# Kernel tuning notes

Hardware: AMD Instinct MI355X
Metric: run time of the kernel (lower is better)

The kernel has to match this reference:

```python
import jax, jax.numpy as jnp
import numpy as np

B, S, H, NH, HD = 2, 2048, 1024, 16, 64
THETA = 10000.0


def setup_inputs() -> dict:
    key = jax.random.key(0)
    k1, k2, k3, k4, k5 = jax.random.split(key, 5)
    hidden_states = jax.random.normal(k1, (B, S, H), dtype=jnp.float32)
    # RoPE tables, interleaved-pair layout: [c0,c0,c1,c1,...] along head_dim
    inv_freq = 1.0 / (THETA ** (jnp.arange(0, HD, 2, dtype=jnp.float32) / HD))
    t = jnp.arange(S, dtype=jnp.float32)
    freqs = jnp.outer(t, inv_freq)                      # [S, HD//2]
    freqs_cos = jnp.repeat(jnp.cos(freqs), 2, axis=-1)  # [S, HD]
    freqs_sin = jnp.repeat(jnp.sin(freqs), 2, axis=-1)  # [S, HD]
    position_ids = jnp.arange(S, dtype=jnp.int32)
    w = 0.02
    Wq = jax.random.normal(k2, (H, H), dtype=jnp.float32) * w
    Wk = jax.random.normal(k3, (H, H), dtype=jnp.float32) * w
    Wv = jax.random.normal(k4, (H, H), dtype=jnp.float32) * w
    Wo = jax.random.normal(k5, (H, H), dtype=jnp.float32) * w
    return {"hidden_states": hidden_states, "freqs_cos": freqs_cos,
            "freqs_sin": freqs_sin, "position_ids": position_ids,
            "Wq": Wq, "Wk": Wk, "Wv": Wv, "Wo": Wo}


def _rotate_half_interleaved(x):
    # stack([-x[..., 1::2], x[..., ::2]], -1).reshape_as(x)
    xe = x.reshape(x.shape[:-1] + (HD // 2, 2))
    return jnp.stack([-xe[..., 1], xe[..., 0]], axis=-1).reshape(x.shape)


def reference(hidden_states, freqs_cos, freqs_sin, position_ids, Wq, Wk, Wv, Wo):
    b, s, _ = hidden_states.shape
    # QKV projections (torch Linear: y = x @ W.T), split into heads [b, nh, s, hd]
    q = jnp.einsum('bsh,oh->bso', hidden_states, Wq).reshape(b, s, NH, HD).transpose(0, 2, 1, 3)
    k = jnp.einsum('bsh,oh->bso', hidden_states, Wk).reshape(b, s, NH, HD).transpose(0, 2, 1, 3)
    v = jnp.einsum('bsh,oh->bso', hidden_states, Wv).reshape(b, s, NH, HD).transpose(0, 2, 1, 3)
    cos = freqs_cos[position_ids][None, None]  # [1, 1, s, hd]
    sin = freqs_sin[position_ids][None, None]
    rq = _rotate_half_interleaved(q)
    # NOTE: faithful to source bug — rotate_half_k is built from q, not k
    q = q * cos + rq * sin
    k = k * cos + rq * sin
    # causal SDPA, scale = 1/sqrt(head_dim)
    scores = jnp.einsum('bhqd,bhkd->bhqk', q, k) / jnp.sqrt(jnp.float32(HD))
    causal = jnp.tril(jnp.ones((s, s), dtype=bool))
    scores = jnp.where(causal, scores, jnp.float32(-1e30))
    attn = jax.nn.softmax(scores, axis=-1)
    out = jnp.einsum('bhqk,bhkd->bhqd', attn, v)
    out = out.transpose(0, 2, 1, 3).reshape(b, s, H)
    return jnp.einsum('bsh,oh->bso', out, Wo)
```

## Files before the change

kernel.cpp:

```cpp
#include <hip/hip_runtime.h>
#include <stdint.h>

#define BB 2
#define SS 2048
#define HH 1024
#define NHH 16
#define HDD 64

typedef short bf16s;
typedef __attribute__((ext_vector_type(8))) short short8;
typedef __attribute__((ext_vector_type(4))) short short4v;
typedef __attribute__((ext_vector_type(2))) short short2v;
typedef __attribute__((ext_vector_type(4))) float f32x4;
typedef _Float16 half4v __attribute__((ext_vector_type(4)));
typedef _Float16 half8v __attribute__((ext_vector_type(8)));
typedef __fp16 fp16x2 __attribute__((ext_vector_type(2)));

__device__ inline short f2bf(float f) {
  union { float f; uint32_t u; } v; v.f = f;
  uint32_t r = (v.u + 0x7fffu + ((v.u >> 16) & 1u)) >> 16;
  return (short)r;
}
__device__ inline float bf2f(short h) {
  union { uint32_t u; float f; } v; v.u = ((uint32_t)(uint16_t)h) << 16;
  return v.f;
}

__device__ __forceinline__ float exp2_raw(float x) {
  float r;
  asm("v_exp_f32 %0, %1\n\ts_nop 0" : "=v"(r) : "v"(x));
  return r;
}

__device__ inline void gld_lds16(const void* g, void* l) {
  __builtin_amdgcn_global_load_lds((const __attribute__((address_space(1))) void*)g,
                                   (__attribute__((address_space(3))) void*)l, 16, 0, 0);
}

__device__ inline void stv(short* C, size_t i, float v) { C[i] = f2bf(v); }
__device__ inline void stv(float* C, size_t i, float v) { C[i] = v; }

__device__ inline f32x4 mfma_k32(short8 a, short8 b, f32x4 c) {
  return __builtin_amdgcn_mfma_f32_16x16x32_bf16(a, b, c, 0, 0, 0);
}
__device__ inline f32x4 mfma_k32(half8v a, half8v b, f32x4 c) {
  return __builtin_amdgcn_mfma_f32_16x16x32_f16(a, b, c, 0, 0, 0);
}
template <typename ET> struct ftr;
template <> struct ftr<short>     { using v8 = short8; };
template <> struct ftr<_Float16>  { using v8 = half8v; };

__global__ __launch_bounds__(256) void convert_all(
    const float* __restrict__ x, const float* __restrict__ Wq,
    const float* __restrict__ Wk, const float* __restrict__ Wv,
    const float* __restrict__ Wo, bf16s* __restrict__ xb,
    bf16s* __restrict__ wqkv, _Float16* __restrict__ wof) {
  const long M1 = 1024L * 1024L;
  long e = (long)(blockIdx.x * blockDim.x + threadIdx.x) * 4;
  if (e < 7 * M1) {
    const float* src; bf16s* dst;
    if (e < 4 * M1)      { src = x  + e;            dst = xb   + e; }
    else if (e < 5 * M1) { src = Wq + (e - 4 * M1); dst = wqkv + (e - 4 * M1); }
    else if (e < 6 * M1) { src = Wk + (e - 5 * M1); dst = wqkv + (e - 4 * M1); }
    else                 { src = Wv + (e - 6 * M1); dst = wqkv + (e - 4 * M1); }
    float4 v = *(const float4*)src;
    short4v o;
    o.x = f2bf(v.x); o.y = f2bf(v.y); o.z = f2bf(v.z); o.w = f2bf(v.w);
    *(short4v*)dst = o;
  } else {
    float4 v = *(const float4*)(Wo + (e - 7 * M1));
    half4v o;
    o.x = (_Float16)v.x; o.y = (_Float16)v.y;
    o.z = (_Float16)v.z; o.w = (_Float16)v.w;
    *(half4v*)(wof + (e - 7 * M1)) = o;
  }
}

template <typename ET, typename OT, int MT>
__global__ __launch_bounds__(256) void gemm_bt(
    const ET* __restrict__ A, const ET* __restrict__ Bm,
    OT* __restrict__ C, int K, int ldc) {
  using V8 = typename ftr<ET>::v8;
  __shared__ __align__(16) ET As[MT * 32 * 64];
  __shared__ __align__(16) ET Bs[128 * 64];
  const int tid = threadIdx.x;
  const int lane = tid & 63, w = tid >> 6;
  const int quad = lane >> 4, mcol = lane & 15;
  const int bm = blockIdx.y * (MT * 32), bn = blockIdx.x * 128;
  const int wm = (w >> 1) * (MT * 16), wn = (w & 1) * 64;
  f32x4 acc[MT][4] = {};
  const int nkt = K >> 6;
  for (int kt = 0; kt < nkt; ++kt) {
    __syncthreads();
#pragma unroll
    for (int i = 0; i < MT; ++i) {
      int seg = (i * 4 + w) * 512;
      int flat = seg + lane * 8;
      int row = flat >> 6;
      int cpos = (flat >> 3) & 7;
      int cs = cpos ^ (row & 7);
      gld_lds16(A + (size_t)(bm + row) * K + kt * 64 + cs * 8, &As[seg]);
    }
#pragma unroll
    for (int i = 0; i < 4; ++i) {
      int seg = (i * 4 + w) * 512;
      int flat = seg + lane * 8;
      int row = flat >> 6;
      int cpos = (flat >> 3) & 7;
      int cs = cpos ^ (row & 7);
      gld_lds16(Bm + (size_t)(bn + row) * K + kt * 64 + cs * 8, &Bs[seg]);
    }
    __syncthreads();
#pragma unroll
    for (int ks = 0; ks < 2; ++ks) {
      V8 af[MT], bf[4];
#pragma unroll
      for (int mt = 0; mt < MT; ++mt) {
        int row = wm + mt * 16 + mcol;
        int cs = (ks * 4 + quad) ^ (row & 7);
        af[mt] = *(const V8*)&As[row * 64 + cs * 8];
      }
#pragma unroll
      for (int nt = 0; nt < 4; ++nt) {
        int row = wn + nt * 16 + mcol;
        int cs = (ks * 4 + quad) ^ (row & 7);
        bf[nt] = *(const V8*)&Bs[row * 64 + cs * 8];
      }
#pragma unroll
      for (int mt = 0; mt < MT; ++mt)
#pragma unroll
        for (int nt = 0; nt < 4; ++nt)
          acc[mt][nt] = mfma_k32(af[mt], bf[nt], acc[mt][nt]);
    }
  }
#pragma unroll
  for (int mt = 0; mt < MT; ++mt)
#pragma unroll
    for (int nt = 0; nt < 4; ++nt) {
      int r0 = bm + wm + mt * 16 + quad * 4;
      int c = bn + wn + nt * 16 + mcol;
#pragma unroll
      for (int r = 0; r < 4; ++r)
        stv(C, (size_t)(r0 + r) * ldc + c, acc[mt][nt][r]);
    }
}

__global__ __launch_bounds__(256) void postproc(
    const bf16s* __restrict__ qkv, const float* __restrict__ fcos,
    const float* __restrict__ fsin, const int* __restrict__ pos,
    bf16s* __restrict__ Q, bf16s* __restrict__ Kc, _Float16* __restrict__ Vt) {
  const float LOG2E = 1.4426950408889634f;
  const int st = blockIdx.x, bh = blockIdx.y;
  const int b = bh >> 4, h = bh & 15;
  const int tid = threadIdx.x;
  const int m0 = b * 2048 + st * 64;
  {
    const int row = tid >> 2, pc = tid & 3;
    const int s = st * 64 + row;
    const int p = pos[s];
    const bf16s* qp = qkv + (size_t)(m0 + row) * 3072 + h * 64 + pc * 16;
    short8 qv[2] = { *(const short8*)qp, *(const short8*)(qp + 8) };
    short8 kv[2] = { *(const short8*)(qp + 1024), *(const short8*)(qp + 1032) };
    const float* cp = fcos + (size_t)p * 64 + pc * 16;
    const float* sp = fsin + (size_t)p * 64 + pc * 16;
    short8 qo[2], ko[2];
#pragma unroll
    for (int hf = 0; hf < 2; ++hf)
#pragma unroll
      for (int j = 0; j < 4; ++j) {
        float c = cp[hf * 8 + 2 * j], sn = sp[hf * 8 + 2 * j];
        float q0 = bf2f(qv[hf][2 * j]), q1 = bf2f(qv[hf][2 * j + 1]);
        float k0 = bf2f(kv[hf][2 * j]), k1 = bf2f(kv[hf][2 * j + 1]);
        qo[hf][2 * j]     = f2bf((q0 * c - q1 * sn) * 0.125f);
        qo[hf][2 * j + 1] = f2bf((q1 * c + q0 * sn) * 0.125f);
        ko[hf][2 * j]     = f2bf((k0 * c - q1 * sn) * LOG2E);
        ko[hf][2 * j + 1] = f2bf((k1 * c + q0 * sn) * LOG2E);
      }
    size_t o = ((size_t)bh * 2048 + s) * 64 + pc * 16;
    *(short8*)&Q[o] = qo[0];  *(short8*)&Q[o + 8] = qo[1];
    *(short8*)&Kc[o] = ko[0]; *(short8*)&Kc[o + 8] = ko[1];
  }
  __shared__ __align__(16) _Float16 T[64 * 72];
#pragma unroll
  for (int p2 = 0; p2 < 2; ++p2) {
    int sl = p2 * 32 + (tid >> 3);
    int ch = tid & 7;
    short8 v = *(const short8*)&qkv[(size_t)(m0 + sl) * 3072 + 2048 + h * 64 + ch * 8];
#pragma unroll
    for (int j = 0; j < 8; ++j) T[(ch * 8 + j) * 72 + sl] = (_Float16)bf2f(v[j]);
  }
  __syncthreads();
#pragma unroll
  for (int p2 = 0; p2 < 2; ++p2) {
    int dl = p2 * 32 + (tid >> 3);
    int ch = tid & 7;
    half8v v = *(const half8v*)&T[dl * 72 + ch * 8];
    *(half8v*)&Vt[((size_t)bh * 64 + dl) * 2048 + st * 64 + ch * 8] = v;
  }
}

template <bool DOB>
__device__ __forceinline__ void step2(
    const bf16s* __restrict__ Ks, const _Float16* __restrict__ Vp,
    const short8* bqA, const short8* bqB,
    f32x4* OA, f32x4* OB, float& lA, float& lB,
    bool diagA, bool diagB, int w, int quad, int col) {
  f32x4 sA[4], sB[4];
#pragma unroll
  for (int t = 0; t < 4; ++t) {
    f32x4 a = {}, bb = {};
#pragma unroll
    for (int ks = 0; ks < 2; ++ks) {
      int krow = t * 16 + col;
      int cs = (ks * 4 + quad) ^ (krow & 7);
      short8 af = *(const short8*)&Ks[krow * 64 + cs * 8];
      a = __builtin_amdgcn_mfma_f32_16x16x32_bf16(af, bqA[ks], a, 0, 0, 0);
      if (DOB) bb = __builtin_amdgcn_mfma_f32_16x16x32_bf16(af, bqB[ks], bb, 0, 0, 0);
    }
    sA[t] = a;
    if (DOB) sB[t] = bb;
  }
  if (diagA) {
#pragma unroll
    for (int t = 0; t < 4; ++t)
#pragma unroll
      for (int r = 0; r < 4; ++r)
        if (t * 16 + quad * 4 + r > w * 16 + col) sA[t][r] = -1e30f;
  }
  if (DOB && diagB) {
#pragma unroll
    for (int t = 0; t < 4; ++t)
#pragma unroll
      for (int r = 0; r < 4; ++r)
        if (t * 16 + quad * 4 + r > w * 16 + col) sB[t][r] = -1e30f;
  }
  half4v paA[4], paB[4];
#pragma unroll
  for (int t = 0; t < 4; ++t) {
    {
      float p0 = exp2_raw(sA[t][0]), p1 = exp2_raw(sA[t][1]);
      float p2 = exp2_raw(sA[t][2]), p3 = exp2_raw(sA[t][3]);
      lA += (p0 + p1) + (p2 + p3);
      union { fp16x2 h2[2]; half4v h4; } u;
      u.h2[0] = __builtin_amdgcn_cvt_pkrtz(p0, p1);
      u.h2[1] = __builtin_amdgcn_cvt_pkrtz(p2, p3);
      paA[t] = u.h4;
    }
    if (DOB) {
      float p0 = exp2_raw(sB[t][0]), p1 = exp2_raw(sB[t][1]);
      float p2 = exp2_raw(sB[t][2]), p3 = exp2_raw(sB[t][3]);
      lB += (p0 + p1) + (p2 + p3);
      union { fp16x2 h2[2]; half4v h4; } u;
      u.h2[0] = __builtin_amdgcn_cvt_pkrtz(p0, p1);
      u.h2[1] = __builtin_amdgcn_cvt_pkrtz(p2, p3);
      paB[t] = u.h4;
    }
  }
#pragma unroll
  for (int dt = 0; dt < 4; ++dt) {
    int vrow = dt * 16 + col;
    const _Float16* vp = &Vp[vrow * 72 + (quad ^ (vrow & 3)) * 16];
    union { half8v v8; half4v v4[2]; } a01, a23;
    a01.v8 = *(const half8v*)vp;
    a23.v8 = *(const half8v*)(vp + 8);
    half4v bv[4] = { a01.v4[0], a01.v4[1], a23.v4[0], a23.v4[1] };
#pragma unroll
    for (int t = 0; t < 4; ++t) {
      OA[dt] = __builtin_amdgcn_mfma_f32_16x16x16f16(paA[t], bv[t], OA[dt], 0, 0, 0);
      if (DOB) OB[dt] = __builtin_amdgcn_mfma_f32_16x16x16f16(paB[t], bv[t], OB[dt], 0, 0, 0);
    }
  }
}

__global__ __launch_bounds__(256) void attn(
    const bf16s* __restrict__ Q, const bf16s* __restrict__ Kb,
    const _Float16* __restrict__ Vt, _Float16* __restrict__ O) {
  __shared__ __align__(16) bf16s Ks[2][64 * 64];
  __shared__ __align__(16) _Float16 Vp[2][64 * 72];
  const int bh = blockIdx.y;
  const int tid = threadIdx.x, lane = tid & 63, w = tid >> 6;
  const int quad = lane >> 4, col = lane & 15;
  const size_t base = (size_t)bh * 2048 * 64;
  const _Float16* vbase = Vt + (size_t)bh * 64 * 2048;
  const int b = bh >> 4, h = bh & 15;
  const int x = blockIdx.x;
  const int qbA = 31 - x, qbB = x;

  short8 bqA[2], bqB[2];
  {
    const int qrA = qbA * 64 + w * 16 + col;
    const int qrB = qbB * 64 + w * 16 + col;
#pragma unroll
    for (int ks = 0; ks < 2; ++ks) {
      bqA[ks] = *(const short8*)&Q[base + (size_t)qrA * 64 + ks * 32 + quad * 8];
      bqB[ks] = *(const short8*)&Q[base + (size_t)qrB * 64 + ks * 32 + quad * 8];
    }
  }
  f32x4 OA[4] = {}, OB[4] = {};
  float lA = 0.f, lB = 0.f;

  const int vd = tid >> 2, vc = tid & 3;
  const int rot = vd & 3;

  {
    half8v vr0 = *(const half8v*)&vbase[(size_t)vd * 2048 + vc * 16];
    half8v vr1 = *(const half8v*)&vbase[(size_t)vd * 2048 + vc * 16 + 8];
#pragma unroll
    for (int i = 0; i < 2; ++i) {
      int seg = (i * 4 + w) * 512;
      int flat = seg + lane * 8;
      int row = flat >> 6, cpos = (flat >> 3) & 7;
      int cs = cpos ^ (row & 7);
      gld_lds16(&Kb[base + (size_t)row * 64 + cs * 8], &Ks[0][seg]);
    }
    union { half8v v8; half4v v4[2]; } u0, u1;
    u0.v8 = vr0; u1.v8 = vr1;
    int rbase = vd * 72 + vc * 4;
    *(half4v*)&Vp[0][rbase + (0 ^ rot) * 16] = u0.v4[0];
    *(half4v*)&Vp[0][rbase + (1 ^ rot) * 16] = u0.v4[1];
    *(half4v*)&Vp[0][rbase + (2 ^ rot) * 16] = u1.v4[0];
    *(half4v*)&Vp[0][rbase + (3 ^ rot) * 16] = u1.v4[1];
    __syncthreads();
  }

  for (int kt = 0; kt <= qbA; ++kt) {
    const int cur = kt & 1, nxt = cur ^ 1;
    const bool pf = (kt < qbA);
    half8v vr0, vr1;
    if (pf) {
      vr0 = *(const half8v*)&vbase[(size_t)vd * 2048 + (kt + 1) * 64 + vc * 16];
      vr1 = *(const half8v*)&vbase[(size_t)vd * 2048 + (kt + 1) * 64 + vc * 16 + 8];
#pragma unroll
      for (int i = 0; i < 2; ++i) {
        int seg = (i * 4 + w) * 512;
        int flat = seg + lane * 8;
        int row = flat >> 6, cpos = (flat >> 3) & 7;
        int cs = cpos ^ (row & 7);
        gld_lds16(&Kb[base + (size_t)((kt + 1) * 64 + row) * 64 + cs * 8],
                  &Ks[nxt][seg]);
      }
    }
    if (kt <= qbB)
      step2<true>(Ks[cur], Vp[cur], bqA, bqB, OA, OB, lA, lB,
                  false, kt == qbB, w, quad, col);
    else
      step2<false>(Ks[cur], Vp[cur], bqA, bqB, OA, OB, lA, lB,
                   kt == qbA, false, w, quad, col);
    if (pf) {
      union { half8v v8; half4v v4[2]; } u0, u1;
      u0.v8 = vr0; u1.v8 = vr1;
      int rbase = vd * 72 + vc * 4;
      *(half4v*)&Vp[nxt][rbase + (0 ^ rot) * 16] = u0.v4[0];
      *(half4v*)&Vp[nxt][rbase + (1 ^ rot) * 16] = u0.v4[1];
      *(half4v*)&Vp[nxt][rbase + (2 ^ rot) * 16] = u1.v4[0];
      *(half4v*)&Vp[nxt][rbase + (3 ^ rot) * 16] = u1.v4[1];
    }
    __syncthreads();
  }

  lA += __shfl_xor(lA, 16); lA += __shfl_xor(lA, 32);
  lB += __shfl_xor(lB, 16); lB += __shfl_xor(lB, 32);

#pragma unroll
  for (int which = 0; which < 2; ++which) {
    const int qb = which ? qbB : qbA;
    const f32x4* Oacc = which ? OB : OA;
    const float l = which ? lB : lA;
    float l4[4];
#pragma unroll
    for (int r = 0; r < 4; ++r) l4[r] = __shfl(l, quad * 4 + r);
#pragma unroll
    for (int dt = 0; dt < 4; ++dt)
#pragma unroll
      for (int r = 0; r < 4; ++r) {
        int srow = qb * 64 + w * 16 + quad * 4 + r;
        O[((size_t)b * 2048 + srow) * 1024 + h * 64 + dt * 16 + col] =
            (_Float16)(Oacc[dt][r] / l4[r]);
      }
  }
}

extern "C" void kernel_launch(void* const* d_in, const int* in_sizes, int n_in,
                              void* d_out, int out_size, void* d_ws, size_t ws_size,
                              hipStream_t stream) {
  (void)in_sizes; (void)n_in; (void)out_size; (void)ws_size;
  const float* x  = (const float*)d_in[0];
  const float* fc = (const float*)d_in[1];
  const float* fs = (const float*)d_in[2];
  const int* pos  = (const int*)d_in[3];
  const float* Wq = (const float*)d_in[4];
  const float* Wk = (const float*)d_in[5];
  const float* Wv = (const float*)d_in[6];
  const float* Wo = (const float*)d_in[7];
  float* out = (float*)d_out;
  char* ws = (char*)d_ws;
  const size_t MB = 1024 * 1024;
  bf16s* xb    = (bf16s*)(ws);
  bf16s* wqkv  = (bf16s*)(ws + 8 * MB);
  _Float16* wof = (_Float16*)(ws + 14 * MB);
  bf16s* qkv   = (bf16s*)(ws + 16 * MB);
  bf16s* Qb    = (bf16s*)(ws + 40 * MB);
  bf16s* Kb    = (bf16s*)(ws + 48 * MB);
  _Float16* Vt = (_Float16*)(ws + 56 * MB);
  _Float16* Ob = (_Float16*)(ws);

  convert_all<<<8192, 256, 0, stream>>>(x, Wq, Wk, Wv, Wo, xb, wqkv, wof);
  gemm_bt<short, short, 4><<<dim3(24, 32), 256, 0, stream>>>(xb, wqkv, qkv, 1024, 3072);
  postproc<<<dim3(32, 32), 256, 0, stream>>>(qkv, fc, fs, pos, Qb, Kb, Vt);
  attn<<<dim3(16, 32), 256, 0, stream>>>(Qb, Kb, Vt, Ob);
  gemm_bt<_Float16, float, 2><<<dim3(8, 64), 256, 0, stream>>>(Ob, wof, out, 1024, 1024);
}
```

Before: 197.4 us.

## Split attention KV loop across two wave groups with LDS reduction

```diff
diff --git a/kernel.cpp b/kernel.cpp
--- a/kernel.cpp
+++ b/kernel.cpp
@@ -272,14 +272,19 @@
   }
 }
 
-__global__ __launch_bounds__(256) void attn(
+__global__ __launch_bounds__(512, 4) void attn(
     const bf16s* __restrict__ Q, const bf16s* __restrict__ Kb,
     const _Float16* __restrict__ Vt, _Float16* __restrict__ O) {
-  __shared__ __align__(16) bf16s Ks[2][64 * 64];
-  __shared__ __align__(16) _Float16 Vp[2][64 * 72];
+  __shared__ __align__(16) bf16s KsAll[2][2][64 * 64];
+  __shared__ __align__(16) _Float16 VpAll[2][2][64 * 72];
   const int bh = blockIdx.y;
-  const int tid = threadIdx.x, lane = tid & 63, w = tid >> 6;
+  const int tid = threadIdx.x;
+  const int w8 = tid >> 6;
+  const int g = w8 >> 2;
+  const int w = w8 & 3;
+  const int lane = tid & 63;
   const int quad = lane >> 4, col = lane & 15;
+  const int ltid = tid & 255;
   const size_t base = (size_t)bh * 2048 * 64;
   const _Float16* vbase = Vt + (size_t)bh * 64 * 2048;
   const int b = bh >> 4, h = bh & 15;
@@ -299,84 +304,112 @@
   f32x4 OA[4] = {}, OB[4] = {};
   float lA = 0.f, lB = 0.f;
 
-  const int vd = tid >> 2, vc = tid & 3;
+  const int vd = ltid >> 2, vc = ltid & 3;
   const int rot = vd & 3;
+  const int nsteps = qbA + 1;
 
   {
-    half8v vr0 = *(const half8v*)&vbase[(size_t)vd * 2048 + vc * 16];
-    half8v vr1 = *(const half8v*)&vbase[(size_t)vd * 2048 + vc * 16 + 8];
+    half8v vr0 = *(const half8v*)&vbase[(size_t)vd * 2048 + g * 64 + vc * 16];
+    half8v vr1 = *(const half8v*)&vbase[(size_t)vd * 2048 + g * 64 + vc * 16 + 8];
 #pragma unroll
     for (int i = 0; i < 2; ++i) {
       int seg = (i * 4 + w) * 512;
       int flat = seg + lane * 8;
       int row = flat >> 6, cpos = (flat >> 3) & 7;
       int cs = cpos ^ (row & 7);
-      gld_lds16(&Kb[base + (size_t)row * 64 + cs * 8], &Ks[0][seg]);
+      gld_lds16(&Kb[base + (size_t)(g * 64 + row) * 64 + cs * 8], &KsAll[g][0][seg]);
     }
     union { half8v v8; half4v v4[2]; } u0, u1;
     u0.v8 = vr0; u1.v8 = vr1;
     int rbase = vd * 72 + vc * 4;
-    *(half4v*)&Vp[0][rbase + (0 ^ rot) * 16] = u0.v4[0];
-    *(half4v*)&Vp[0][rbase + (1 ^ rot) * 16] = u0.v4[1];
-    *(half4v*)&Vp[0][rbase + (2 ^ rot) * 16] = u1.v4[0];
-    *(half4v*)&Vp[0][rbase + (3 ^ rot) * 16] = u1.v4[1];
+    *(half4v*)&VpAll[g][0][rbase + (0 ^ rot) * 16] = u0.v4[0];
+    *(half4v*)&VpAll[g][0][rbase + (1 ^ rot) * 16] = u0.v4[1];
+    *(half4v*)&VpAll[g][0][rbase + (2 ^ rot) * 16] = u1.v4[0];
+    *(half4v*)&VpAll[g][0][rbase + (3 ^ rot) * 16] = u1.v4[1];
     __syncthreads();
   }
 
-  for (int kt = 0; kt <= qbA; ++kt) {
-    const int cur = kt & 1, nxt = cur ^ 1;
-    const bool pf = (kt < qbA);
+  const int nit = (nsteps + 1) >> 1;
+  for (int it = 0; it < nit; ++it) {
+    const int kt = 2 * it + g;
+    const int cur = it & 1, nxt = cur ^ 1;
+    const bool act = (kt < nsteps);
+    const bool pf = (kt + 2 < nsteps);
     half8v vr0, vr1;
     if (pf) {
-      vr0 = *(const half8v*)&vbase[(size_t)vd * 2048 + (kt + 1) * 64 + vc * 16];
-      vr1 = *(const half8v*)&vbase[(size_t)vd * 2048 + (kt + 1) * 64 + vc * 16 + 8];
+      vr0 = *(const half8v*)&vbase[(size_t)vd * 2048 + (kt + 2) * 64 + vc * 16];
+      vr1 = *(const half8v*)&vbase[(size_t)vd * 2048 + (kt + 2) * 64 + vc * 16 + 8];
 #pragma unroll
       for (int i = 0; i < 2; ++i) {
         int seg = (i * 4 + w) * 512;
         int flat = seg + lane * 8;
         int row = flat >> 6, cpos = (flat >> 3) & 7;
         int cs = cpos ^ (row & 7);
-        gld_lds16(&Kb[base + (size_t)((kt + 1) * 64 + row) * 64 + cs * 8],
-                  &Ks[nxt][seg]);
+        gld_lds16(&Kb[base + (size_t)((kt + 2) * 64 + row) * 64 + cs * 8],
+                  &KsAll[g][nxt][seg]);
       }
     }
-    if (kt <= qbB)
-      step2<true>(Ks[cur], Vp[cur], bqA, bqB, OA, OB, lA, lB,
-                  false, kt == qbB, w, quad, col);
-    else
-      step2<false>(Ks[cur], Vp[cur], bqA, bqB, OA, OB, lA, lB,
-                   kt == qbA, false, w, quad, col);
+    if (act) {
+      if (kt <= qbB)
+        step2<true>(KsAll[g][cur], VpAll[g][cur], bqA, bqB, OA, OB, lA, lB,
+                    false, kt == qbB, w, quad, col);
+      else
+        step2<false>(KsAll[g][cur], VpAll[g][cur], bqA, bqB, OA, OB, lA, lB,
+                     kt == qbA, false, w, quad, col);
+    }
     if (pf) {
       union { half8v v8; half4v v4[2]; } u0, u1;
       u0.v8 = vr0; u1.v8 = vr1;
       int rbase = vd * 72 + vc * 4;
-      *(half4v*)&Vp[nxt][rbase + (0 ^ rot) * 16] = u0.v4[0];
-      *(half4v*)&Vp[nxt][rbase + (1 ^ rot) * 16] = u0.v4[1];
-      *(half4v*)&Vp[nxt][rbase + (2 ^ rot) * 16] = u1.v4[0];
-      *(half4v*)&Vp[nxt][rbase + (3 ^ rot) * 16] = u1.v4[1];
+      *(half4v*)&VpAll[g][nxt][rbase + (0 ^ rot) * 16] = u0.v4[0];
+      *(half4v*)&VpAll[g][nxt][rbase + (1 ^ rot) * 16] = u0.v4[1];
+      *(half4v*)&VpAll[g][nxt][rbase + (2 ^ rot) * 16] = u1.v4[0];
+      *(half4v*)&VpAll[g][nxt][rbase + (3 ^ rot) * 16] = u1.v4[1];
     }
     __syncthreads();
   }
 
-  lA += __shfl_xor(lA, 16); lA += __shfl_xor(lA, 32);
-  lB += __shfl_xor(lB, 16); lB += __shfl_xor(lB, 32);
-
-#pragma unroll
-  for (int which = 0; which < 2; ++which) {
-    const int qb = which ? qbB : qbA;
-    const f32x4* Oacc = which ? OB : OA;
-    const float l = which ? lB : lA;
-    float l4[4];
-#pragma unroll
-    for (int r = 0; r < 4; ++r) l4[r] = __shfl(l, quad * 4 + r);
-#pragma unroll
-    for (int dt = 0; dt < 4; ++dt)
-#pragma unroll
-      for (int r = 0; r < 4; ++r) {
-        int srow = qb * 64 + w * 16 + quad * 4 + r;
-        O[((size_t)b * 2048 + srow) * 1024 + h * 64 + dt * 16 + col] =
-            (_Float16)(Oacc[dt][r] / l4[r]);
-      }
+  float* dOA = (float*)&KsAll[0][0][0];
+  float* dOB = (float*)&VpAll[0][0][0];
+  float* dl  = (float*)&VpAll[0][0][0] + 4096;
+  const int t4 = w * 64 + lane;
+  if (g == 1) {
+#pragma unroll
+    for (int dt = 0; dt < 4; ++dt) {
+      *(f32x4*)&dOA[t4 * 16 + dt * 4] = OA[dt];
+      *(f32x4*)&dOB[t4 * 16 + dt * 4] = OB[dt];
+    }
+    dl[t4 * 2] = lA; dl[t4 * 2 + 1] = lB;
+  }
+  __syncthreads();
+  if (g == 0) {
+#pragma unroll
+    for (int dt = 0; dt < 4; ++dt) {
+      OA[dt] += *(const f32x4*)&dOA[t4 * 16 + dt * 4];
+      OB[dt] += *(const f32x4*)&dOB[t4 * 16 + dt * 4];
+    }
+    lA += dl[t4 * 2]; lB += dl[t4 * 2 + 1];
+
+    lA += __shfl_xor(lA, 16); lA += __shfl_xor(lA, 32);
+    lB += __shfl_xor(lB, 16); lB += __shfl_xor(lB, 32);
+
+#pragma unroll
+    for (int which = 0; which < 2; ++which) {
+      const int qb = which ? qbB : qbA;
+      const f32x4* Oacc = which ? OB : OA;
+      const float l = which ? lB : lA;
+      float l4[4];
+#pragma unroll
+      for (int r = 0; r < 4; ++r) l4[r] = __shfl(l, quad * 4 + r);
+#pragma unroll
+      for (int dt = 0; dt < 4; ++dt)
+#pragma unroll
+        for (int r = 0; r < 4; ++r) {
+          int srow = qb * 64 + w * 16 + quad * 4 + r;
+          O[((size_t)b * 2048 + srow) * 1024 + h * 64 + dt * 16 + col] =
+              (_Float16)(Oacc[dt][r] / l4[r]);
+        }
+    }
   }
 }
 
@@ -407,6 +440,6 @@
   convert_all<<<8192, 256, 0, stream>>>(x, Wq, Wk, Wv, Wo, xb, wqkv, wof);
   gemm_bt<short, short, 4><<<dim3(24, 32), 256, 0, stream>>>(xb, wqkv, qkv, 1024, 3072);
   postproc<<<dim3(32, 32), 256, 0, stream>>>(qkv, fc, fs, pos, Qb, Kb, Vt);
-  attn<<<dim3(16, 32), 256, 0, stream>>>(Qb, Kb, Vt, Ob);
+  attn<<<dim3(16, 32), 512, 0, stream>>>(Qb, Kb, Vt, Ob);
   gemm_bt<_Float16, float, 2><<<dim3(8, 64), 256, 0, stream>>>(Ob, wof, out, 1024, 1024);
 }
```

Result: no change. 196.0 us (-0.7%).

## Process 128-key tiles per attention iteration and fuse causal mask into score loop

Applied to the files above, without the earlier changes.

```diff
diff --git a/kernel.cpp b/kernel.cpp
--- a/kernel.cpp
+++ b/kernel.cpp
@@ -204,10 +204,10 @@
     const bf16s* __restrict__ Ks, const _Float16* __restrict__ Vp,
     const short8* bqA, const short8* bqB,
     f32x4* OA, f32x4* OB, float& lA, float& lB,
-    bool diagA, bool diagB, int w, int quad, int col) {
-  f32x4 sA[4], sB[4];
-#pragma unroll
-  for (int t = 0; t < 4; ++t) {
+    bool diagA, bool diagB, int doffA, int doffB, int quad, int col) {
+  half4v paA[8], paB[8];
+#pragma unroll
+  for (int t = 0; t < 8; ++t) {
     f32x4 a = {}, bb = {};
 #pragma unroll
     for (int ks = 0; ks < 2; ++ks) {
@@ -217,29 +217,14 @@
       a = __builtin_amdgcn_mfma_f32_16x16x32_bf16(af, bqA[ks], a, 0, 0, 0);
       if (DOB) bb = __builtin_amdgcn_mfma_f32_16x16x32_bf16(af, bqB[ks], bb, 0, 0, 0);
     }
-    sA[t] = a;
-    if (DOB) sB[t] = bb;
-  }
-  if (diagA) {
-#pragma unroll
-    for (int t = 0; t < 4; ++t)
+    if (diagA) {
 #pragma unroll
       for (int r = 0; r < 4; ++r)
-        if (t * 16 + quad * 4 + r > w * 16 + col) sA[t][r] = -1e30f;
-  }
-  if (DOB && diagB) {
-#pragma unroll
-    for (int t = 0; t < 4; ++t)
-#pragma unroll
-      for (int r = 0; r < 4; ++r)
-        if (t * 16 + quad * 4 + r > w * 16 + col) sB[t][r] = -1e30f;
-  }
-  half4v paA[4], paB[4];
-#pragma unroll
-  for (int t = 0; t < 4; ++t) {
+        if (t * 16 + quad * 4 + r > doffA) a[r] = -1e30f;
+    }
     {
-      float p0 = exp2_raw(sA[t][0]), p1 = exp2_raw(sA[t][1]);
-      float p2 = exp2_raw(sA[t][2]), p3 = exp2_raw(sA[t][3]);
+      float p0 = exp2_raw(a[0]), p1 = exp2_raw(a[1]);
+      float p2 = exp2_raw(a[2]), p3 = exp2_raw(a[3]);
       lA += (p0 + p1) + (p2 + p3);
       union { fp16x2 h2[2]; half4v h4; } u;
       u.h2[0] = __builtin_amdgcn_cvt_pkrtz(p0, p1);
@@ -247,8 +232,13 @@
       paA[t] = u.h4;
     }
     if (DOB) {
-      float p0 = exp2_raw(sB[t][0]), p1 = exp2_raw(sB[t][1]);
-      float p2 = exp2_raw(sB[t][2]), p3 = exp2_raw(sB[t][3]);
+      if (diagB) {
+#pragma unroll
+        for (int r = 0; r < 4; ++r)
+          if (t * 16 + quad * 4 + r > doffB) bb[r] = -1e30f;
+      }
+      float p0 = exp2_raw(bb[0]), p1 = exp2_raw(bb[1]);
+      float p2 = exp2_raw(bb[2]), p3 = exp2_raw(bb[3]);
       lB += (p0 + p1) + (p2 + p3);
       union { fp16x2 h2[2]; half4v h4; } u;
       u.h2[0] = __builtin_amdgcn_cvt_pkrtz(p0, p1);
@@ -259,13 +249,16 @@
 #pragma unroll
   for (int dt = 0; dt < 4; ++dt) {
     int vrow = dt * 16 + col;
-    const _Float16* vp = &Vp[vrow * 72 + (quad ^ (vrow & 3)) * 16];
-    union { half8v v8; half4v v4[2]; } a01, a23;
-    a01.v8 = *(const half8v*)vp;
-    a23.v8 = *(const half8v*)(vp + 8);
-    half4v bv[4] = { a01.v4[0], a01.v4[1], a23.v4[0], a23.v4[1] };
-#pragma unroll
-    for (int t = 0; t < 4; ++t) {
+    int voff = vrow * 72 + (quad ^ (vrow & 3)) * 16;
+    union { half8v v8; half4v v4[2]; } a01, a23, b01, b23;
+    a01.v8 = *(const half8v*)&Vp[voff];
+    a23.v8 = *(const half8v*)&Vp[voff + 8];
+    b01.v8 = *(const half8v*)&Vp[4608 + voff];
+    b23.v8 = *(const half8v*)&Vp[4608 + voff + 8];
+    half4v bv[8] = { a01.v4[0], a01.v4[1], a23.v4[0], a23.v4[1],
+                     b01.v4[0], b01.v4[1], b23.v4[0], b23.v4[1] };
+#pragma unroll
+    for (int t = 0; t < 8; ++t) {
       OA[dt] = __builtin_amdgcn_mfma_f32_16x16x16f16(paA[t], bv[t], OA[dt], 0, 0, 0);
       if (DOB) OB[dt] = __builtin_amdgcn_mfma_f32_16x16x16f16(paB[t], bv[t], OB[dt], 0, 0, 0);
     }
@@ -275,8 +268,8 @@
 __global__ __launch_bounds__(256) void attn(
     const bf16s* __restrict__ Q, const bf16s* __restrict__ Kb,
     const _Float16* __restrict__ Vt, _Float16* __restrict__ O) {
-  __shared__ __align__(16) bf16s Ks[2][64 * 64];
-  __shared__ __align__(16) _Float16 Vp[2][64 * 72];
+  __shared__ __align__(16) bf16s Ks[2][128 * 64];
+  __shared__ __align__(16) _Float16 Vp[2][2][64 * 72];
   const int bh = blockIdx.y;
   const int tid = threadIdx.x, lane = tid & 63, w = tid >> 6;
   const int quad = lane >> 4, col = lane & 15;
@@ -301,59 +294,75 @@
 
   const int vd = tid >> 2, vc = tid & 3;
   const int rot = vd & 3;
+  const int nkt = (qbA >> 1) + 1;
+  const int nkB = qbB >> 1;
+  const int doffA = w * 16 + col + ((qbA & 1) << 6);
+  const int doffB = w * 16 + col + ((qbB & 1) << 6);
 
   {
-    half8v vr0 = *(const half8v*)&vbase[(size_t)vd * 2048 + vc * 16];
-    half8v vr1 = *(const half8v*)&vbase[(size_t)vd * 2048 + vc * 16 + 8];
-#pragma unroll
-    for (int i = 0; i < 2; ++i) {
+#pragma unroll
+    for (int i = 0; i < 4; ++i) {
       int seg = (i * 4 + w) * 512;
       int flat = seg + lane * 8;
       int row = flat >> 6, cpos = (flat >> 3) & 7;
       int cs = cpos ^ (row & 7);
       gld_lds16(&Kb[base + (size_t)row * 64 + cs * 8], &Ks[0][seg]);
     }
-    union { half8v v8; half4v v4[2]; } u0, u1;
-    u0.v8 = vr0; u1.v8 = vr1;
     int rbase = vd * 72 + vc * 4;
-    *(half4v*)&Vp[0][rbase + (0 ^ rot) * 16] = u0.v4[0];
-    *(half4v*)&Vp[0][rbase + (1 ^ rot) * 16] = u0.v4[1];
-    *(half4v*)&Vp[0][rbase + (2 ^ rot) * 16] = u1.v4[0];
-    *(half4v*)&Vp[0][rbase + (3 ^ rot) * 16] = u1.v4[1];
+#pragma unroll
+    for (int j = 0; j < 2; ++j) {
+      half8v r0 = *(const half8v*)&vbase[(size_t)vd * 2048 + j * 64 + vc * 16];
+      half8v r1 = *(const half8v*)&vbase[(size_t)vd * 2048 + j * 64 + vc * 16 + 8];
+      union { half8v v8; half4v v4[2]; } u0, u1;
+      u0.v8 = r0; u1.v8 = r1;
+      *(half4v*)&Vp[0][j][rbase + (0 ^ rot) * 16] = u0.v4[0];
+      *(half4v*)&Vp[0][j][rbase + (1 ^ rot) * 16] = u0.v4[1];
+      *(half4v*)&Vp[0][j][rbase + (2 ^ rot) * 16] = u1.v4[0];
+      *(half4v*)&Vp[0][j][rbase + (3 ^ rot) * 16] = u1.v4[1];
+    }
     __syncthreads();
   }
 
-  for (int kt = 0; kt <= qbA; ++kt) {
-    const int cur = kt & 1, nxt = cur ^ 1;
-    const bool pf = (kt < qbA);
-    half8v vr0, vr1;
+  for (int kt2 = 0; kt2 < nkt; ++kt2) {
+    const int cur = kt2 & 1, nxt = cur ^ 1;
+    const bool pf = (kt2 + 1 < nkt);
+    half8v v00, v01, v10, v11;
     if (pf) {
-      vr0 = *(const half8v*)&vbase[(size_t)vd * 2048 + (kt + 1) * 64 + vc * 16];
-      vr1 = *(const half8v*)&vbase[(size_t)vd * 2048 + (kt + 1) * 64 + vc * 16 + 8];
-#pragma unroll
-      for (int i = 0; i < 2; ++i) {
+      const size_t vo = (size_t)vd * 2048 + (kt2 + 1) * 128 + vc * 16;
+      v00 = *(const half8v*)&vbase[vo];
+      v01 = *(const half8v*)&vbase[vo + 8];
+      v10 = *(const half8v*)&vbase[vo + 64];
+      v11 = *(const half8v*)&vbase[vo + 72];
+#pragma unroll
+      for (int i = 0; i < 4; ++i) {
         int seg = (i * 4 + w) * 512;
         int flat = seg + lane * 8;
         int row = flat >> 6, cpos = (flat >> 3) & 7;
         int cs = cpos ^ (row & 7);
-        gld_lds16(&Kb[base + (size_t)((kt + 1) * 64 + row) * 64 + cs * 8],
+        gld_lds16(&Kb[base + (size_t)((kt2 + 1) * 128 + row) * 64 + cs * 8],
                   &Ks[nxt][seg]);
       }
     }
-    if (kt <= qbB)
-      step2<true>(Ks[cur], Vp[cur], bqA, bqB, OA, OB, lA, lB,
-                  false, kt == qbB, w, quad, col);
+    const bool dA = (kt2 == nkt - 1);
+    if (kt2 <= nkB)
+      step2<true>(Ks[cur], &Vp[cur][0][0], bqA, bqB, OA, OB, lA, lB,
+                  dA, kt2 == nkB, doffA, doffB, quad, col);
     else
-      step2<false>(Ks[cur], Vp[cur], bqA, bqB, OA, OB, lA, lB,
-                   kt == qbA, false, w, quad, col);
+      step2<false>(Ks[cur], &Vp[cur][0][0], bqA, bqB, OA, OB, lA, lB,
+                   dA, false, doffA, doffB, quad, col);
     if (pf) {
+      int rbase = vd * 72 + vc * 4;
       union { half8v v8; half4v v4[2]; } u0, u1;
-      u0.v8 = vr0; u1.v8 = vr1;
-      int rbase = vd * 72 + vc * 4;
-      *(half4v*)&Vp[nxt][rbase + (0 ^ rot) * 16] = u0.v4[0];
-      *(half4v*)&Vp[nxt][rbase + (1 ^ rot) * 16] = u0.v4[1];
-      *(half4v*)&Vp[nxt][rbase + (2 ^ rot) * 16] = u1.v4[0];
-      *(half4v*)&Vp[nxt][rbase + (3 ^ rot) * 16] = u1.v4[1];
+      u0.v8 = v00; u1.v8 = v01;
+      *(half4v*)&Vp[nxt][0][rbase + (0 ^ rot) * 16] = u0.v4[0];
+      *(half4v*)&Vp[nxt][0][rbase + (1 ^ rot) * 16] = u0.v4[1];
+      *(half4v*)&Vp[nxt][0][rbase + (2 ^ rot) * 16] = u1.v4[0];
+      *(half4v*)&Vp[nxt][0][rbase + (3 ^ rot) * 16] = u1.v4[1];
+      u0.v8 = v10; u1.v8 = v11;
+      *(half4v*)&Vp[nxt][1][rbase + (0 ^ rot) * 16] = u0.v4[0];
+      *(half4v*)&Vp[nxt][1][rbase + (1 ^ rot) * 16] = u0.v4[1];
+      *(half4v*)&Vp[nxt][1][rbase + (2 ^ rot) * 16] = u1.v4[0];
+      *(half4v*)&Vp[nxt][1][rbase + (3 ^ rot) * 16] = u1.v4[1];
     }
     __syncthreads();
   }
```

After: 218.2 us. 1.11x slower.

## Process four causal query blocks per attention workgroup with shared K/V tiles

Applied to the files above, without the earlier changes.

```diff
diff --git a/kernel.cpp b/kernel.cpp
--- a/kernel.cpp
+++ b/kernel.cpp
@@ -199,61 +199,51 @@
   }
 }
 
-template <bool DOB>
-__device__ __forceinline__ void step2(
+__device__ __forceinline__ void step4(
     const bf16s* __restrict__ Ks, const _Float16* __restrict__ Vp,
-    const short8* bqA, const short8* bqB,
-    f32x4* OA, f32x4* OB, float& lA, float& lB,
-    bool diagA, bool diagB, int w, int quad, int col) {
-  f32x4 sA[4], sB[4];
-#pragma unroll
-  for (int t = 0; t < 4; ++t) {
-    f32x4 a = {}, bb = {};
+    const short8 (&bq)[4][2], f32x4 (&Oa)[4][4], float (&l)[4],
+    const int (&qb)[4], int kt, int w, int quad, int col) {
+  short8 afr[4][2];
+#pragma unroll
+  for (int t = 0; t < 4; ++t)
 #pragma unroll
     for (int ks = 0; ks < 2; ++ks) {
       int krow = t * 16 + col;
       int cs = (ks * 4 + quad) ^ (krow & 7);
-      short8 af = *(const short8*)&Ks[krow * 64 + cs * 8];
-      a = __builtin_amdgcn_mfma_f32_16x16x32_bf16(af, bqA[ks], a, 0, 0, 0);
-      if (DOB) bb = __builtin_amdgcn_mfma_f32_16x16x32_bf16(af, bqB[ks], bb, 0, 0, 0);
-    }
-    sA[t] = a;
-    if (DOB) sB[t] = bb;
-  }
-  if (diagA) {
-#pragma unroll
-    for (int t = 0; t < 4; ++t)
-#pragma unroll
-      for (int r = 0; r < 4; ++r)
-        if (t * 16 + quad * 4 + r > w * 16 + col) sA[t][r] = -1e30f;
-  }
-  if (DOB && diagB) {
-#pragma unroll
-    for (int t = 0; t < 4; ++t)
-#pragma unroll
-      for (int r = 0; r < 4; ++r)
-        if (t * 16 + quad * 4 + r > w * 16 + col) sB[t][r] = -1e30f;
-  }
-  half4v paA[4], paB[4];
-#pragma unroll
-  for (int t = 0; t < 4; ++t) {
-    {
-      float p0 = exp2_raw(sA[t][0]), p1 = exp2_raw(sA[t][1]);
-      float p2 = exp2_raw(sA[t][2]), p3 = exp2_raw(sA[t][3]);
-      lA += (p0 + p1) + (p2 + p3);
-      union { fp16x2 h2[2]; half4v h4; } u;
-      u.h2[0] = __builtin_amdgcn_cvt_pkrtz(p0, p1);
-      u.h2[1] = __builtin_amdgcn_cvt_pkrtz(p2, p3);
-      paA[t] = u.h4;
-    }
-    if (DOB) {
-      float p0 = exp2_raw(sB[t][0]), p1 = exp2_raw(sB[t][1]);
-      float p2 = exp2_raw(sB[t][2]), p3 = exp2_raw(sB[t][3]);
-      lB += (p0 + p1) + (p2 + p3);
-      union { fp16x2 h2[2]; half4v h4; } u;
-      u.h2[0] = __builtin_amdgcn_cvt_pkrtz(p0, p1);
-      u.h2[1] = __builtin_amdgcn_cvt_pkrtz(p2, p3);
-      paB[t] = u.h4;
+      afr[t][ks] = *(const short8*)&Ks[krow * 64 + cs * 8];
+    }
+  half4v pa[4][4];
+#pragma unroll
+  for (int j = 0; j < 4; ++j) {
+    if (kt <= qb[j]) {
+      f32x4 s[4];
+      __builtin_amdgcn_s_setprio(1);
+#pragma unroll
+      for (int t = 0; t < 4; ++t) {
+        f32x4 a = {};
+#pragma unroll
+        for (int ks = 0; ks < 2; ++ks)
+          a = __builtin_amdgcn_mfma_f32_16x16x32_bf16(afr[t][ks], bq[j][ks], a, 0, 0, 0);
+        s[t] = a;
+      }
+      __builtin_amdgcn_s_setprio(0);
+      if (kt == qb[j]) {
+#pragma unroll
+        for (int t = 0; t < 4; ++t)
+#pragma unroll
+          for (int r = 0; r < 4; ++r)
+            if (t * 16 + quad * 4 + r > w * 16 + col) s[t][r] = -1e30f;
+      }
+#pragma unroll
+      for (int t = 0; t < 4; ++t) {
+        float p0 = exp2_raw(s[t][0]), p1 = exp2_raw(s[t][1]);
+        float p2 = exp2_raw(s[t][2]), p3 = exp2_raw(s[t][3]);
+        l[j] += (p0 + p1) + (p2 + p3);
+        union { fp16x2 h2[2]; half4v h4; } u;
+        u.h2[0] = __builtin_amdgcn_cvt_pkrtz(p0, p1);
+        u.h2[1] = __builtin_amdgcn_cvt_pkrtz(p2, p3);
+        pa[j][t] = u.h4;
+      }
     }
   }
 #pragma unroll
@@ -264,15 +254,18 @@
     a01.v8 = *(const half8v*)vp;
     a23.v8 = *(const half8v*)(vp + 8);
     half4v bv[4] = { a01.v4[0], a01.v4[1], a23.v4[0], a23.v4[1] };
-#pragma unroll
-    for (int t = 0; t < 4; ++t) {
-      OA[dt] = __builtin_amdgcn_mfma_f32_16x16x16f16(paA[t], bv[t], OA[dt], 0, 0, 0);
-      if (DOB) OB[dt] = __builtin_amdgcn_mfma_f32_16x16x16f16(paB[t], bv[t], OB[dt], 0, 0, 0);
-    }
-  }
-}
-
-__global__ __launch_bounds__(256) void attn(
+    __builtin_amdgcn_s_setprio(1);
+#pragma unroll
+    for (int t = 0; t < 4; ++t)
+#pragma unroll
+      for (int j = 0; j < 4; ++j)
+        if (kt <= qb[j])
+          Oa[j][dt] = __builtin_amdgcn_mfma_f32_16x16x16f16(pa[j][t], bv[t], Oa[j][dt], 0, 0, 0);
+    __builtin_amdgcn_s_setprio(0);
+  }
+}
+
+__global__ __launch_bounds__(256, 1) void attn(
     const bf16s* __restrict__ Q, const bf16s* __restrict__ Kb,
     const _Float16* __restrict__ Vt, _Float16* __restrict__ O) {
   __shared__ __align__(16) bf16s Ks[2][64 * 64];
@@ -284,20 +277,19 @@
   const _Float16* vbase = Vt + (size_t)bh * 64 * 2048;
   const int b = bh >> 4, h = bh & 15;
   const int x = blockIdx.x;
-  const int qbA = 31 - x, qbB = x;
-
-  short8 bqA[2], bqB[2];
-  {
-    const int qrA = qbA * 64 + w * 16 + col;
-    const int qrB = qbB * 64 + w * 16 + col;
-#pragma unroll
-    for (int ks = 0; ks < 2; ++ks) {
-      bqA[ks] = *(const short8*)&Q[base + (size_t)qrA * 64 + ks * 32 + quad * 8];
-      bqB[ks] = *(const short8*)&Q[base + (size_t)qrB * 64 + ks * 32 + quad * 8];
-    }
-  }
-  f32x4 OA[4] = {}, OB[4] = {};
-  float lA = 0.f, lB = 0.f;
+  const int qb[4] = { x, 15 - x, 16 + x, 31 - x };
+  const int nsteps = 32 - x;
+
+  short8 bq[4][2];
+#pragma unroll
+  for (int j = 0; j < 4; ++j) {
+    const int qr = qb[j] * 64 + w * 16 + col;
+#pragma unroll
+    for (int ks = 0; ks < 2; ++ks)
+      bq[j][ks] = *(const short8*)&Q[base + (size_t)qr * 64 + ks * 32 + quad * 8];
+  }
+  f32x4 Oa[4][4] = {};
+  float l[4] = {};
 
   const int vd = tid >> 2, vc = tid & 3;
   const int rot = vd & 3;
@@ -323,9 +315,9 @@
     __syncthreads();
   }
 
-  for (int kt = 0; kt <= qbA; ++kt) {
+  for (int kt = 0; kt < nsteps; ++kt) {
     const int cur = kt & 1, nxt = cur ^ 1;
-    const bool pf = (kt < qbA);
+    const bool pf = (kt + 1 < nsteps);
     half8v vr0, vr1;
     if (pf) {
       vr0 = *(const half8v*)&vbase[(size_t)vd * 2048 + (kt + 1) * 64 + vc * 16];
@@ -340,12 +332,7 @@
                   &Ks[nxt][seg]);
       }
     }
-    if (kt <= qbB)
-      step2<true>(Ks[cur], Vp[cur], bqA, bqB, OA, OB, lA, lB,
-                  false, kt == qbB, w, quad, col);
-    else
-      step2<false>(Ks[cur], Vp[cur], bqA, bqB, OA, OB, lA, lB,
-                   kt == qbA, false, w, quad, col);
+    step4(Ks[cur], Vp[cur], bq, Oa, l, qb, kt, w, quad, col);
     if (pf) {
       union { half8v v8; half4v v4[2]; } u0, u1;
       u0.v8 = vr0; u1.v8 = vr1;
@@ -358,24 +345,20 @@
     __syncthreads();
   }
 
-  lA += __shfl_xor(lA, 16); lA += __shfl_xor(lA, 32);
-  lB += __shfl_xor(lB, 16); lB += __shfl_xor(lB, 32);
-
-#pragma unroll
-  for (int which = 0; which < 2; ++which) {
-    const int qb = which ? qbB : qbA;
-    const f32x4* Oacc = which ? OB : OA;
-    const float l = which ? lB : lA;
+#pragma unroll
+  for (int j = 0; j < 4; ++j) {
+    float lj = l[j];
+    lj += __shfl_xor(lj, 16); lj += __shfl_xor(lj, 32);
     float l4[4];
 #pragma unroll
-    for (int r = 0; r < 4; ++r) l4[r] = __shfl(l, quad * 4 + r);
+    for (int r = 0; r < 4; ++r) l4[r] = __shfl(lj, quad * 4 + r);
 #pragma unroll
     for (int dt = 0; dt < 4; ++dt)
 #pragma unroll
       for (int r = 0; r < 4; ++r) {
-        int srow = qb * 64 + w * 16 + quad * 4 + r;
+        int srow = qb[j] * 64 + w * 16 + quad * 4 + r;
         O[((size_t)b * 2048 + srow) * 1024 + h * 64 + dt * 16 + col] =
-            (_Float16)(Oacc[dt][r] / l4[r]);
+            (_Float16)(Oa[j][dt][r] / l4[r]);
       }
   }
 }
@@ -407,6 +390,6 @@
   convert_all<<<8192, 256, 0, stream>>>(x, Wq, Wk, Wv, Wo, xb, wqkv, wof);
   gemm_bt<short, short, 4><<<dim3(24, 32), 256, 0, stream>>>(xb, wqkv, qkv, 1024, 3072);
   postproc<<<dim3(32, 32), 256, 0, stream>>>(qkv, fc, fs, pos, Qb, Kb, Vt);
-  attn<<<dim3(16, 32), 256, 0, stream>>>(Qb, Kb, Vt, Ob);
+  attn<<<dim3(8, 32), 256, 0, stream>>>(Qb, Kb, Vt, Ob);
   gemm_bt<_Float16, float, 2><<<dim3(8, 64), 256, 0, stream>>>(Ob, wof, out, 1024, 1024);
 }
```

Measured after the change: 215.1 us. +9.0%, slower.
